# Kernel optimization log

Measured on AMD Instinct MI355X. Metric: run time of the kernel, lower is better.

Reference implementation:

```python
import jax, jax.numpy as jnp
import numpy as np

B, T, D, H, HS = 256, 256, 384, 6, 64  # batch, seq (=block_size), n_embd, n_heads, head_size


def setup_inputs() -> dict:
    key = jax.random.key(0)
    k0, k1, k2 = jax.random.split(key, 3)
    x = jax.random.normal(k0, (B, T, D), dtype=jnp.float32)
    # per-head qkv weights, stacked: [H, n_embd, 3*head_size] (x @ W layout)
    W_qkv = jax.random.normal(k1, (H, D, 3 * HS), dtype=jnp.float32) * 0.02
    W_out = jax.random.normal(k2, (H * HS, D), dtype=jnp.float32) * 0.02
    b_out = jnp.zeros((D,), dtype=jnp.float32)
    return {"x": x, "W_qkv": W_qkv, "W_out": W_out, "b_out": b_out}


def reference(x, W_qkv, W_out, b_out):
    # Eval-mode (dropout disabled). Vectorized over heads instead of the
    # original Python loop; identical math per head.
    b, t, d = x.shape
    h, hs3 = W_qkv.shape[0], W_qkv.shape[2]
    hs = hs3 // 3
    qkv = jnp.einsum('btd,hde->bhte', x, W_qkv)  # [B,H,T,3*HS]
    q, k, v = jnp.split(qkv, 3, axis=-1)  # each [B,H,T,HS]
    scale = 1.0 / jnp.sqrt(jnp.asarray(hs, dtype=x.dtype))
    wei = jnp.einsum('bhte,bhse->bhts', q, k) * scale  # [B,H,T,T]
    causal = jnp.tril(jnp.ones((t, t), dtype=bool))
    wei = jnp.where(causal, wei, -jnp.inf)
    wei = jax.nn.softmax(wei, axis=-1)
    out = jnp.einsum('bhts,bhse->bhte', wei, v)  # [B,H,T,HS]
    out = out.transpose(0, 2, 1, 3).reshape(b, t, h * hs)  # concat heads
    return out @ W_out + b_out
```

## Files before the change

### kernel.cpp

```cpp
#include <hip/hip_runtime.h>


typedef __attribute__((ext_vector_type(8))) short short8;
typedef __attribute__((ext_vector_type(4))) float f32x4;

#define NBATCH 256
#define NT 256
#define ND 384
#define NH 6
#define NHS 64

__device__ __forceinline__ unsigned short f2bf(float f) {
  unsigned int u = __float_as_uint(f);
  u += 0x7fffu + ((u >> 16) & 1u);
  return (unsigned short)(u >> 16);
}

__device__ __forceinline__ ushort4 pack4(f32x4 v) {
  ushort4 p;
  p.x = f2bf(v[0]); p.y = f2bf(v[1]); p.z = f2bf(v[2]); p.w = f2bf(v[3]);
  return p;
}

__device__ __forceinline__ unsigned int cvtpk(float lo, float hi) {
  unsigned int r;
  asm("v_cvt_pk_bf16_f32 %0, %1, %2" : "=v"(r) : "v"(lo), "v"(hi));
  return r;
}

__device__ __forceinline__ void gload16(const void* g, void* l) {
  __builtin_amdgcn_global_load_lds(
      (const __attribute__((address_space(1))) void*)g,
      (__attribute__((address_space(3))) void*)l, 16, 0, 0);
}

__global__ __launch_bounds__(256) void x_to_bf16(const float* __restrict__ x,
                                                 unsigned short* __restrict__ xb) {
  size_t i = ((size_t)blockIdx.x * 256 + threadIdx.x) * 8;
  float4 a = *reinterpret_cast<const float4*>(&x[i]);
  float4 b = *reinterpret_cast<const float4*>(&x[i + 4]);
  ushort4 lo, hi;
  lo.x = f2bf(a.x); lo.y = f2bf(a.y); lo.z = f2bf(a.z); lo.w = f2bf(a.w);
  hi.x = f2bf(b.x); hi.y = f2bf(b.y); hi.z = f2bf(b.z); hi.w = f2bf(b.w);
  *reinterpret_cast<ushort4*>(&xb[i]) = lo;
  *reinterpret_cast<ushort4*>(&xb[i + 4]) = hi;
}

__global__ __launch_bounds__(256) void prep_wqkv(const float* __restrict__ W,
                                                 unsigned short* __restrict__ Wt) {
  int idx = blockIdx.x * 256 + threadIdx.x;
  int h = idx / (192 * ND);
  int rem = idx % (192 * ND);
  int e = rem / ND;
  int d = rem % ND;
  float v = W[((size_t)h * ND + d) * 192 + e];
  if (e < 64) v *= 0.125f * 1.44269504088896340736f;
  Wt[idx] = f2bf(v);
}

__global__ __launch_bounds__(256) void prep_wout(const float* __restrict__ W,
                                                 unsigned short* __restrict__ Wt) {
  int idx = blockIdx.x * 256 + threadIdx.x;
  int n = idx / ND;
  int k = idx % ND;
  Wt[idx] = f2bf(W[(size_t)k * ND + n]);
}

__global__ __launch_bounds__(256, 2) void qkv_gemm(const unsigned short* __restrict__ xb,
                                                   const unsigned short* __restrict__ Wt,
                                                   unsigned short* __restrict__ Qb,
                                                   unsigned short* __restrict__ Kb,
                                                   unsigned short* __restrict__ Vtb) {
  __shared__ __align__(16) unsigned short As[2][128 * 64];
  __shared__ __align__(16) unsigned short Bs[2][192 * 64];
  const int tid = threadIdx.x;
  const int lane = tid & 63, w = tid >> 6;
  const int l15 = lane & 15, lg = lane >> 4;
  const int wm = w >> 1, wn = w & 1;

  const int bid = blockIdx.x;
  const int xcd = bid & 7, pos = bid >> 3;
  const int h = pos % 6;
  const int mt = xcd * 64 + pos / 6;
  const int m0 = mt * 128;
  const unsigned short* Wh = Wt + (size_t)h * 192 * ND;

  f32x4 acc[4][6];
#pragma unroll
  for (int i = 0; i < 4; i++)
#pragma unroll
    for (int j = 0; j < 6; j++) acc[i][j] = (f32x4){0.f, 0.f, 0.f, 0.f};

  int arow[4], acsw[4], brow[6], bcsw[6];
#pragma unroll
  for (int j = 0; j < 4; j++) {
    int chunk = j * 256 + tid;
    arow[j] = chunk >> 3;
    acsw[j] = (chunk & 7) ^ (arow[j] & 7);
  }
#pragma unroll
  for (int j = 0; j < 6; j++) {
    int chunk = j * 256 + tid;
    brow[j] = chunk >> 3;
    bcsw[j] = (chunk & 7) ^ (brow[j] & 7);
  }

#define STAGE(nb, k0)                                                              \
  do {                                                                             \
    _Pragma("unroll") for (int j = 0; j < 4; j++)                                  \
        gload16(&xb[(size_t)(m0 + arow[j]) * ND + (k0) + acsw[j] * 8],             \
                &As[nb][(j * 256 + w * 64) * 8]);                                  \
    _Pragma("unroll") for (int j = 0; j < 6; j++)                                  \
        gload16(&Wh[(size_t)brow[j] * ND + (k0) + bcsw[j] * 8],                    \
                &Bs[nb][(j * 256 + w * 64) * 8]);                                  \
  } while (0)

  STAGE(0, 0);
  __syncthreads();

  int cur = 0;
  for (int kt = 0; kt < 6; ++kt) {
    if (kt < 5) STAGE(cur ^ 1, (kt + 1) * 64);
    short8 af[4][2], bf[6][2];
#pragma unroll
    for (int mi = 0; mi < 4; mi++) {
      const int row = wm * 64 + mi * 16 + l15;
#pragma unroll
      for (int kk = 0; kk < 2; kk++)
        af[mi][kk] = *reinterpret_cast<const short8*>(
            &As[cur][row * 64 + (((kk * 4 + lg) ^ (row & 7)) * 8)]);
    }
#pragma unroll
    for (int ni = 0; ni < 6; ni++) {
      const int row = wn * 96 + ni * 16 + l15;
#pragma unroll
      for (int kk = 0; kk < 2; kk++)
        bf[ni][kk] = *reinterpret_cast<const short8*>(
            &Bs[cur][row * 64 + (((kk * 4 + lg) ^ (row & 7)) * 8)]);
    }
#pragma unroll
    for (int kk = 0; kk < 2; kk++)
#pragma unroll
      for (int mi = 0; mi < 4; mi++)
#pragma unroll
        for (int ni = 0; ni < 6; ni++)
          acc[mi][ni] = __builtin_amdgcn_mfma_f32_16x16x32_bf16(af[mi][kk], bf[ni][kk], acc[mi][ni], 0, 0, 0);
    __syncthreads();
    cur ^= 1;
  }

  const int b = m0 >> 8, t0 = m0 & 255;
  const size_t bh = (size_t)b * NH + h;
#pragma unroll
  for (int mi = 0; mi < 4; mi++)
#pragma unroll
    for (int ni = 0; ni < 6; ni++) {
      const int col = wn * 96 + ni * 16 + l15;
      const int p = col >> 6, e = col & 63;
      const int mr = wm * 64 + mi * 16 + lg * 4;
      if (p == 2) {
        *reinterpret_cast<ushort4*>(&Vtb[(bh * 64 + e) * NT + t0 + mr]) = pack4(acc[mi][ni]);
      } else {
        unsigned short* dst = (p == 0) ? Qb : Kb;
        size_t base = (bh * NT + t0 + mr) * 64 + e;
#pragma unroll
        for (int r = 0; r < 4; r++) dst[base + (size_t)r * 64] = f2bf(acc[mi][ni][r]);
      }
    }
#undef STAGE
}

__global__ __launch_bounds__(256, 2) void attn_fwd(const unsigned short* __restrict__ Qb,
                                                   const unsigned short* __restrict__ Kb,
                                                   const unsigned short* __restrict__ Vtb,
                                                   unsigned short* __restrict__ AO) {
  __shared__ __align__(16) unsigned short Ks[256 * 64];
  __shared__ __align__(16) unsigned short Vs[64 * 256];
  __shared__ __align__(16) unsigned short Plds[4][32 * 64];
  const int bh = blockIdx.x;
  const int tid = threadIdx.x;
  const int w = tid >> 6, lane = tid & 63;
  const int l15 = lane & 15, lg = lane >> 4;
  const unsigned short* Qh = Qb + (size_t)bh * NT * 64;
  const unsigned short* Kh = Kb + (size_t)bh * NT * 64;
  const unsigned short* Vh = Vtb + (size_t)bh * 64 * NT;
  unsigned short* P = Plds[w];
  const int swz = (l15 & 7) << 3;

#pragma unroll
  for (int j = 0; j < 8; j++) {
    const int c = j * 256 + tid;
    const int row = c >> 3, cc = c & 7;
    gload16(&Kh[(size_t)row * 64 + ((cc ^ (row & 7)) * 8)], &Ks[c * 8]);
  }
#pragma unroll
  for (int j = 0; j < 8; j++) {
    const int c = j * 256 + tid;
    const int row = c >> 5, cc = c & 31;
    gload16(&Vh[(size_t)row * NT + ((cc ^ (row & 7)) * 8)], &Vs[c * 8]);
  }
  __syncthreads();

  const int b = bh / NH, h = bh % NH;

#pragma unroll
  for (int pass = 0; pass < 2; ++pass) {
    const int qt = pass ? (7 - w) : w;
    const int q0 = qt * 32;

    short8 qf[2][2];
#pragma unroll
    for (int mi = 0; mi < 2; mi++)
#pragma unroll
      for (int kb = 0; kb < 2; kb++)
        qf[mi][kb] = *reinterpret_cast<const short8*>(
            &Qh[(size_t)(q0 + mi * 16 + l15) * 64 + kb * 32 + lg * 8]);

    f32x4 ot[4][2];
#pragma unroll
    for (int i = 0; i < 4; i++)
#pragma unroll
      for (int j = 0; j < 2; j++) ot[i][j] = (f32x4){0.f, 0.f, 0.f, 0.f};
    float mrun[2] = {-3e38f, -3e38f}, lsum[2] = {0.f, 0.f};

    const int nch = (qt >> 1) + 1;
    for (int ch = 0; ch < nch; ++ch) {
      const int kv0 = ch * 64;
      f32x4 st[4][2];
#pragma unroll
      for (int i = 0; i < 4; i++)
#pragma unroll
        for (int j = 0; j < 2; j++) st[i][j] = (f32x4){0.f, 0.f, 0.f, 0.f};
      __builtin_amdgcn_s_setprio(1);
#pragma unroll
      for (int ni = 0; ni < 4; ni++) {
        const int row = kv0 + ni * 16 + l15;
        const short8 kf0 = *reinterpret_cast<const short8*>(
            &Ks[row * 64 + ((lg ^ (row & 7)) * 8)]);
        const short8 kf1 = *reinterpret_cast<const short8*>(
            &Ks[row * 64 + (((4 + lg) ^ (row & 7)) * 8)]);
#pragma unroll
        for (int mi = 0; mi < 2; mi++) {
          st[ni][mi] = __builtin_amdgcn_mfma_f32_16x16x32_bf16(kf0, qf[mi][0], st[ni][mi], 0, 0, 0);
          st[ni][mi] = __builtin_amdgcn_mfma_f32_16x16x32_bf16(kf1, qf[mi][1], st[ni][mi], 0, 0, 0);
        }
      }
      __builtin_amdgcn_s_setprio(0);

      if (ch == nch - 1) {
#pragma unroll
        for (int ni = 0; ni < 4; ni++)
#pragma unroll
          for (int mi = 0; mi < 2; mi++)
#pragma unroll
            for (int r = 0; r < 4; r++)
              if (kv0 + ni * 16 + lg * 4 + r > q0 + mi * 16 + l15)
                st[ni][mi][r] = -1e30f;
      }

#pragma unroll
      for (int mi = 0; mi < 2; mi++) {
        float tmax = st[0][mi][0];
#pragma unroll
        for (int ni = 0; ni < 4; ni++)
#pragma unroll
          for (int r = 0; r < 4; r++) tmax = fmaxf(tmax, st[ni][mi][r]);
        tmax = fmaxf(tmax, __shfl_xor(tmax, 16));
        tmax = fmaxf(tmax, __shfl_xor(tmax, 32));
        if (__any(tmax > mrun[mi] + 8.0f)) {
          const float mnew = fmaxf(mrun[mi], tmax);
          const float corr = __builtin_amdgcn_exp2f(mrun[mi] - mnew);
          lsum[mi] *= corr;
#pragma unroll
          for (int erb = 0; erb < 4; erb++)
#pragma unroll
            for (int r = 0; r < 4; r++) ot[erb][mi][r] *= corr;
          mrun[mi] = mnew;
        }
        const float mref = mrun[mi];
        float ls = 0.f;
        const int prow = (mi * 16 + l15) * 64;
#pragma unroll
        for (int ni = 0; ni < 4; ni++) {
          const float p0 = __builtin_amdgcn_exp2f(st[ni][mi][0] - mref);
          const float p1 = __builtin_amdgcn_exp2f(st[ni][mi][1] - mref);
          const float p2 = __builtin_amdgcn_exp2f(st[ni][mi][2] - mref);
          const float p3 = __builtin_amdgcn_exp2f(st[ni][mi][3] - mref);
          ls += (p0 + p1) + (p2 + p3);
          uint2 wv;
          wv.x = cvtpk(p0, p1);
          wv.y = cvtpk(p2, p3);
          *reinterpret_cast<uint2*>(&P[prow + ((ni * 16 + lg * 4) ^ swz)]) = wv;
        }
        ls += __shfl_xor(ls, 16);
        ls += __shfl_xor(ls, 32);
        lsum[mi] += ls;
      }

      short8 pb[2][2];
#pragma unroll
      for (int kk = 0; kk < 2; kk++)
#pragma unroll
        for (int mi = 0; mi < 2; mi++)
          pb[kk][mi] = *reinterpret_cast<const short8*>(
              &P[(mi * 16 + l15) * 64 + ((kk * 32 + lg * 8) ^ swz)]);
      __builtin_amdgcn_s_setprio(1);
#pragma unroll
      for (int erb = 0; erb < 4; erb++) {
        const int row = erb * 16 + l15;
        const short8 va0 = *reinterpret_cast<const short8*>(
            &Vs[row * 256 + (((ch * 8 + lg) ^ (row & 7)) * 8)]);
        const short8 va1 = *reinterpret_cast<const short8*>(
            &Vs[row * 256 + (((ch * 8 + 4 + lg) ^ (row & 7)) * 8)]);
#pragma unroll
        for (int mi = 0; mi < 2; mi++) {
          ot[erb][mi] = __builtin_amdgcn_mfma_f32_16x16x32_bf16(va0, pb[0][mi], ot[erb][mi], 0, 0, 0);
          ot[erb][mi] = __builtin_amdgcn_mfma_f32_16x16x32_bf16(va1, pb[1][mi], ot[erb][mi], 0, 0, 0);
        }
      }
      __builtin_amdgcn_s_setprio(0);
    }

#pragma unroll
    for (int mi = 0; mi < 2; mi++) {
      const float rl = 1.0f / lsum[mi];
      const int q = q0 + mi * 16 + l15;
#pragma unroll
      for (int erb = 0; erb < 4; erb++) {
        f32x4 v;
#pragma unroll
        for (int r = 0; r < 4; r++) v[r] = ot[erb][mi][r] * rl;
        *reinterpret_cast<ushort4*>(&AO[((size_t)(b * NT + q)) * ND + h * 64 + erb * 16 + lg * 4]) =
            pack4(v);
      }
    }
  }
}

__global__ __launch_bounds__(256) void out_gemm(const unsigned short* __restrict__ AO,
                                                const unsigned short* __restrict__ Wot,
                                                const float* __restrict__ bout,
                                                float* __restrict__ out) {
  __shared__ __align__(16) unsigned short As[128 * 48];
  __shared__ __align__(16) unsigned short Bs[64 * 48];
  const int tid = threadIdx.x;
  const int lane = tid & 63, w = tid >> 6;
  const int l15 = lane & 15, lg = lane >> 4;
  const int wm = w >> 1, wn = w & 1;
  const int n0 = blockIdx.x * 64;
  const int m0 = blockIdx.y * 128;

  f32x4 acc[4][2];
#pragma unroll
  for (int i = 0; i < 4; i++)
#pragma unroll
    for (int j = 0; j < 2; j++) acc[i][j] = (f32x4){0.f, 0.f, 0.f, 0.f};

  const int arow = tid >> 2, ak = (tid & 3) * 8;

  for (int kt = 0; kt < 12; ++kt) {
    const int k0 = kt * 32;
    short8 av0 = *reinterpret_cast<const short8*>(&AO[(size_t)(m0 + arow) * ND + k0 + ak]);
    short8 av1 = *reinterpret_cast<const short8*>(&AO[(size_t)(m0 + 64 + arow) * ND + k0 + ak]);
    short8 bv = *reinterpret_cast<const short8*>(&Wot[(size_t)(n0 + arow) * ND + k0 + ak]);
    __syncthreads();
    *reinterpret_cast<short8*>(&As[arow * 48 + ak]) = av0;
    *reinterpret_cast<short8*>(&As[(64 + arow) * 48 + ak]) = av1;
    *reinterpret_cast<short8*>(&Bs[arow * 48 + ak]) = bv;
    __syncthreads();
    short8 af[4], bf[2];
#pragma unroll
    for (int mi = 0; mi < 4; mi++)
      af[mi] = *reinterpret_cast<const short8*>(&As[(wm * 64 + mi * 16 + l15) * 48 + lg * 8]);
#pragma unroll
    for (int ni = 0; ni < 2; ni++)
      bf[ni] = *reinterpret_cast<const short8*>(&Bs[(wn * 32 + ni * 16 + l15) * 48 + lg * 8]);
#pragma unroll
    for (int mi = 0; mi < 4; mi++)
#pragma unroll
      for (int ni = 0; ni < 2; ni++)
        acc[mi][ni] = __builtin_amdgcn_mfma_f32_16x16x32_bf16(af[mi], bf[ni], acc[mi][ni], 0, 0, 0);
  }

#pragma unroll
  for (int mi = 0; mi < 4; mi++)
#pragma unroll
    for (int ni = 0; ni < 2; ni++) {
      const int c = n0 + wn * 32 + ni * 16 + l15;
      const int mr = m0 + wm * 64 + mi * 16 + lg * 4;
      const float bb = bout[c];
#pragma unroll
      for (int r = 0; r < 4; r++) out[(size_t)(mr + r) * ND + c] = acc[mi][ni][r] + bb;
    }
}

extern "C" void kernel_launch(void* const* d_in, const int* in_sizes, int n_in,
                              void* d_out, int out_size, void* d_ws, size_t ws_size,
                              hipStream_t stream) {
  const float* x = (const float*)d_in[0];
  const float* Wqkv = (const float*)d_in[1];
  const float* Wout = (const float*)d_in[2];
  const float* bout = (const float*)d_in[3];

  char* ws = (char*)d_ws;
  const size_t SZ = (size_t)NBATCH * NH * NT * NHS * 2;
  unsigned short* Qb  = (unsigned short*)(ws);
  unsigned short* Kb  = (unsigned short*)(ws + SZ);
  unsigned short* Vtb = (unsigned short*)(ws + 2 * SZ);
  unsigned short* AO  = (unsigned short*)(ws + 3 * SZ);
  unsigned short* xb  = AO;
  unsigned short* Wqt = (unsigned short*)(ws + 4 * SZ);
  unsigned short* Wot = (unsigned short*)(ws + 4 * SZ + 884736);

  x_to_bf16<<<12288, 256, 0, stream>>>(x, xb);
  prep_wqkv<<<1728, 256, 0, stream>>>(Wqkv, Wqt);
  prep_wout<<<576, 256, 0, stream>>>(Wout, Wot);
  qkv_gemm<<<3072, 256, 0, stream>>>(xb, Wqt, Qb, Kb, Vtb);
  attn_fwd<<<NBATCH * NH, 256, 0, stream>>>(Qb, Kb, Vtb, AO);
  out_gemm<<<dim3(6, 512), 256, 0, stream>>>(AO, Wot, bout, (float*)d_out);
}
```

Baseline: 217.3 us.

## Restructure output GEMM with larger tiles, double-buffered async loads, XCD-aware mapping

Rewrites the output projection GEMM to use 128x192 tiles with a 64-wide K step. Tiles are double-buffered in shared memory and filled through direct global-to-LDS loads (gload16) with an XOR swizzle to avoid bank conflicts. Block indices are remapped so that consecutive M tiles stay on the same XCD, which helps L2 reuse. This removes one barrier per iteration and raises data reuse per block, at the cost of much more LDS (80KB) and more accumulator registers, which can reduce occupancy.

```diff
diff --git a/kernel.cpp b/kernel.cpp
--- a/kernel.cpp
+++ b/kernel.cpp
@@ -337,61 +337,98 @@
   }
 }
 
-__global__ __launch_bounds__(256) void out_gemm(const unsigned short* __restrict__ AO,
-                                                const unsigned short* __restrict__ Wot,
-                                                const float* __restrict__ bout,
-                                                float* __restrict__ out) {
-  __shared__ __align__(16) unsigned short As[128 * 48];
-  __shared__ __align__(16) unsigned short Bs[64 * 48];
+__global__ __launch_bounds__(256, 2) void out_gemm(const unsigned short* __restrict__ AO,
+                                                   const unsigned short* __restrict__ Wot,
+                                                   const float* __restrict__ bout,
+                                                   float* __restrict__ out) {
+  __shared__ __align__(16) unsigned short As[2][128 * 64];
+  __shared__ __align__(16) unsigned short Bs[2][192 * 64];
   const int tid = threadIdx.x;
   const int lane = tid & 63, w = tid >> 6;
   const int l15 = lane & 15, lg = lane >> 4;
   const int wm = w >> 1, wn = w & 1;
-  const int n0 = blockIdx.x * 64;
-  const int m0 = blockIdx.y * 128;
-
-  f32x4 acc[4][2];
+
+  const int bid = blockIdx.x;
+  const int xcd = bid & 7, pos = bid >> 3;
+  const int n0 = (pos & 1) * 192;
+  const int m0 = (xcd * 64 + (pos >> 1)) * 128;
+  const unsigned short* Wh = Wot + (size_t)n0 * ND;
+
+  f32x4 acc[4][6];
 #pragma unroll
   for (int i = 0; i < 4; i++)
 #pragma unroll
-    for (int j = 0; j < 2; j++) acc[i][j] = (f32x4){0.f, 0.f, 0.f, 0.f};
-
-  const int arow = tid >> 2, ak = (tid & 3) * 8;
-
-  for (int kt = 0; kt < 12; ++kt) {
-    const int k0 = kt * 32;
-    short8 av0 = *reinterpret_cast<const short8*>(&AO[(size_t)(m0 + arow) * ND + k0 + ak]);
-    short8 av1 = *reinterpret_cast<const short8*>(&AO[(size_t)(m0 + 64 + arow) * ND + k0 + ak]);
-    short8 bv = *reinterpret_cast<const short8*>(&Wot[(size_t)(n0 + arow) * ND + k0 + ak]);
+    for (int j = 0; j < 6; j++) acc[i][j] = (f32x4){0.f, 0.f, 0.f, 0.f};
+
+  int arow[4], acsw[4], brow[6], bcsw[6];
+#pragma unroll
+  for (int j = 0; j < 4; j++) {
+    int chunk = j * 256 + tid;
+    arow[j] = chunk >> 3;
+    acsw[j] = (chunk & 7) ^ (arow[j] & 7);
+  }
+#pragma unroll
+  for (int j = 0; j < 6; j++) {
+    int chunk = j * 256 + tid;
+    brow[j] = chunk >> 3;
+    bcsw[j] = (chunk & 7) ^ (brow[j] & 7);
+  }
+
+#define STAGE(nb, k0)                                                              \
+  do {                                                                             \
+    _Pragma("unroll") for (int j = 0; j < 4; j++)                                  \
+        gload16(&AO[(size_t)(m0 + arow[j]) * ND + (k0) + acsw[j] * 8],             \
+                &As[nb][(j * 256 + w * 64) * 8]);                                  \
+    _Pragma("unroll") for (int j = 0; j < 6; j++)                                  \
+        gload16(&Wh[(size_t)brow[j] * ND + (k0) + bcsw[j] * 8],                    \
+                &Bs[nb][(j * 256 + w * 64) * 8]);                                  \
+  } while (0)
+
+  STAGE(0, 0);
+  __syncthreads();
+
+  int cur = 0;
+  for (int kt = 0; kt < 6; ++kt) {
+    if (kt < 5) STAGE(cur ^ 1, (kt + 1) * 64);
+    short8 af[4][2], bf[6][2];
+#pragma unroll
+    for (int mi = 0; mi < 4; mi++) {
+      const int row = wm * 64 + mi * 16 + l15;
+#pragma unroll
+      for (int kk = 0; kk < 2; kk++)
+        af[mi][kk] = *reinterpret_cast<const short8*>(
+            &As[cur][row * 64 + (((kk * 4 + lg) ^ (row & 7)) * 8)]);
+    }
+#pragma unroll
+    for (int ni = 0; ni < 6; ni++) {
+      const int row = wn * 96 + ni * 16 + l15;
+#pragma unroll
+      for (int kk = 0; kk < 2; kk++)
+        bf[ni][kk] = *reinterpret_cast<const short8*>(
+            &Bs[cur][row * 64 + (((kk * 4 + lg) ^ (row & 7)) * 8)]);
+    }
+#pragma unroll
+    for (int kk = 0; kk < 2; kk++)
+#pragma unroll
+      for (int mi = 0; mi < 4; mi++)
+#pragma unroll
+        for (int ni = 0; ni < 6; ni++)
+          acc[mi][ni] = __builtin_amdgcn_mfma_f32_16x16x32_bf16(af[mi][kk], bf[ni][kk], acc[mi][ni], 0, 0, 0);
     __syncthreads();
-    *reinterpret_cast<short8*>(&As[arow * 48 + ak]) = av0;
-    *reinterpret_cast<short8*>(&As[(64 + arow) * 48 + ak]) = av1;
-    *reinterpret_cast<short8*>(&Bs[arow * 48 + ak]) = bv;
-    __syncthreads();
-    short8 af[4], bf[2];
-#pragma unroll
-    for (int mi = 0; mi < 4; mi++)
-      af[mi] = *reinterpret_cast<const short8*>(&As[(wm * 64 + mi * 16 + l15) * 48 + lg * 8]);
-#pragma unroll
-    for (int ni = 0; ni < 2; ni++)
-      bf[ni] = *reinterpret_cast<const short8*>(&Bs[(wn * 32 + ni * 16 + l15) * 48 + lg * 8]);
-#pragma unroll
-    for (int mi = 0; mi < 4; mi++)
-#pragma unroll
-      for (int ni = 0; ni < 2; ni++)
-        acc[mi][ni] = __builtin_amdgcn_mfma_f32_16x16x32_bf16(af[mi], bf[ni], acc[mi][ni], 0, 0, 0);
+    cur ^= 1;
   }
 
 #pragma unroll
   for (int mi = 0; mi < 4; mi++)
 #pragma unroll
-    for (int ni = 0; ni < 2; ni++) {
-      const int c = n0 + wn * 32 + ni * 16 + l15;
+    for (int ni = 0; ni < 6; ni++) {
+      const int c = n0 + wn * 96 + ni * 16 + l15;
       const int mr = m0 + wm * 64 + mi * 16 + lg * 4;
       const float bb = bout[c];
 #pragma unroll
       for (int r = 0; r < 4; r++) out[(size_t)(mr + r) * ND + c] = acc[mi][ni][r] + bb;
     }
+#undef STAGE
 }
 
 extern "C" void kernel_launch(void* const* d_in, const int* in_sizes, int n_in,
@@ -417,5 +454,5 @@
   prep_wout<<<576, 256, 0, stream>>>(Wout, Wot);
   qkv_gemm<<<3072, 256, 0, stream>>>(xb, Wqt, Qb, Kb, Vtb);
   attn_fwd<<<NBATCH * NH, 256, 0, stream>>>(Qb, Kb, Vtb, AO);
-  out_gemm<<<dim3(6, 512), 256, 0, stream>>>(AO, Wot, bout, (float*)d_out);
-}
+  out_gemm<<<1024, 256, 0, stream>>>(AO, Wot, bout, (float*)d_out);
+}
```

After: 196.6 us. 1.11x faster.
